# Kernel optimization log

Measured on AMD Instinct MI355X. Metric: run time of the kernel, lower is better.

Reference implementation:

```python
import jax, jax.numpy as jnp
import numpy as np

N_NODES = 100000
N_EDGES = 1200000
IN, HID, OUT = 64, 64, 32


def setup_inputs() -> dict:
    key = jax.random.key(0)
    ks = jax.random.split(key, 8)
    return {
        "features": jax.random.normal(ks[0], (N_NODES, IN), dtype=jnp.float32),
        "src": jax.random.randint(ks[1], (N_EDGES,), 0, N_NODES),
        "dst": jax.random.randint(ks[2], (N_EDGES,), 0, N_NODES),
        "W_self1": jax.random.normal(ks[3], (IN, HID), dtype=jnp.float32) / np.sqrt(IN),
        "W_neigh1": jax.random.normal(ks[4], (IN, HID), dtype=jnp.float32) / np.sqrt(IN),
        "b1": jnp.zeros((HID,), dtype=jnp.float32),
        "W_self2": jax.random.normal(ks[5], (HID, OUT), dtype=jnp.float32) / np.sqrt(HID),
        "W_neigh2": jax.random.normal(ks[6], (HID, OUT), dtype=jnp.float32) / np.sqrt(HID),
        "b2": jnp.zeros((OUT,), dtype=jnp.float32),
    }


def _sage_mean(h, src, dst, n_nodes, W_self, W_neigh, b):
    # DGL SAGEConv(mean): mean over in-neighbors' source features, then
    # rst = fc_self(h_dst) + fc_neigh(h_neigh) + bias
    msg = h[src]  # [E, d] irregular gather
    agg = jax.ops.segment_sum(msg, dst, num_segments=n_nodes)  # [N, d]
    deg = jax.ops.segment_sum(jnp.ones_like(dst, dtype=h.dtype), dst, num_segments=n_nodes)
    h_neigh = agg / jnp.maximum(deg, 1.0)[:, None]  # zero in-degree -> 0 (matches DGL)
    return h @ W_self + h_neigh @ W_neigh + b


def reference(features, src, dst, W_self1, W_neigh1, b1, W_self2, W_neigh2, b2):
    n = features.shape[0]
    # buffer.update is a distributed history-cache passthrough -> identity here
    h = _sage_mean(features, src, dst, n, W_self1, W_neigh1, b1)
    h = _sage_mean(h, src, dst, n, W_self2, W_neigh2, b2)
    return h
```

## Files before the change

### kernel.cpp

```cpp
#include <hip/hip_runtime.h>

constexpr int NN    = 100000;
constexpr int NE    = 1200000;

constexpr int NBUK = 196;
constexpr int PB   = 256;
constexpr int EPB  = (NE + PB - 1) / PB;
constexpr int MAT  = NBUK * PB;
constexpr int NBM  = (NN + 63) / 64;

typedef float  f32x4 __attribute__((ext_vector_type(4)));
typedef short  s16x8 __attribute__((ext_vector_type(8)));

static __device__ __forceinline__ unsigned short f2b(float f) {
    unsigned int u = __float_as_uint(f);
    u = (u + 0x7FFFu + ((u >> 16) & 1u)) >> 16;
    return (unsigned short)u;
}
static __device__ __forceinline__ float blo(unsigned int v) {
    return __uint_as_float(v << 16);
}
static __device__ __forceinline__ float bhi(unsigned int v) {
    return __uint_as_float(v & 0xFFFF0000u);
}

__global__ __launch_bounds__(256) void k_p1hist(const int* __restrict__ dst,
                                                int* __restrict__ mat) {
    __shared__ int h[NBUK];
    const int t = threadIdx.x, blk = blockIdx.x;
    for (int i = t; i < NBUK; i += 256) h[i] = 0;
    __syncthreads();
    int beg4 = blk * (EPB / 4);
    int end4 = beg4 + EPB / 4;
    if (end4 > NE / 4) end4 = NE / 4;
    for (int i = beg4 + t; i < end4; i += 256) {
        const int4 d = ((const int4*)dst)[i];
        atomicAdd(&h[d.x >> 9], 1);
        atomicAdd(&h[d.y >> 9], 1);
        atomicAdd(&h[d.z >> 9], 1);
        atomicAdd(&h[d.w >> 9], 1);
    }
    __syncthreads();
    for (int b = t; b < NBUK; b += 256) mat[b * PB + blk] = h[b];
}

__global__ __launch_bounds__(256) void k_scanA(const int* __restrict__ mat,
                                               int* __restrict__ matX,
                                               int* __restrict__ T) {
    __shared__ int lds[256];
    const int b = blockIdx.x, t = threadIdx.x;
    int v = mat[b * 256 + t];
    lds[t] = v;
    __syncthreads();
    for (int d = 1; d < 256; d <<= 1) {
        int x = (t >= d) ? lds[t - d] : 0;
        __syncthreads();
        lds[t] += x;
        __syncthreads();
    }
    matX[b * 256 + t] = lds[t] - v;
    if (t == 255) T[b] = lds[255];
}

__global__ __launch_bounds__(256) void k_scanB(const int* __restrict__ T,
                                               int* __restrict__ matX) {
    __shared__ int lds[256];
    const int b = blockIdx.x, t = threadIdx.x;
    lds[t] = (t < NBUK) ? T[t] : 0;
    __syncthreads();
    for (int d = 1; d < 256; d <<= 1) {
        int x = (t >= d) ? lds[t - d] : 0;
        __syncthreads();
        lds[t] += x;
        __syncthreads();
    }
    int base = (b == 0) ? 0 : lds[b - 1];
    matX[b * 256 + t] += base;
    if (b == 0 && t == 0) matX[MAT] = NE;
}

__global__ __launch_bounds__(256) void k_p1place(const int* __restrict__ src,
                                                 const int* __restrict__ dst,
                                                 const int* __restrict__ matX,
                                                 unsigned int* __restrict__ P) {
    __shared__ int cur[NBUK];
    const int t = threadIdx.x, blk = blockIdx.x;
    for (int b = t; b < NBUK; b += 256) cur[b] = matX[b * PB + blk];
    __syncthreads();
    int beg4 = blk * (EPB / 4);
    int end4 = beg4 + EPB / 4;
    if (end4 > NE / 4) end4 = NE / 4;
    for (int i = beg4 + t; i < end4; i += 256) {
        const int4 d = ((const int4*)dst)[i];
        const int4 s = ((const int4*)src)[i];
        int p0 = atomicAdd(&cur[d.x >> 9], 1);
        int p1 = atomicAdd(&cur[d.y >> 9], 1);
        int p2 = atomicAdd(&cur[d.z >> 9], 1);
        int p3 = atomicAdd(&cur[d.w >> 9], 1);
        P[p0] = (unsigned)s.x | ((unsigned)(d.x & 511) << 17);
        P[p1] = (unsigned)s.y | ((unsigned)(d.y & 511) << 17);
        P[p2] = (unsigned)s.z | ((unsigned)(d.z & 511) << 17);
        P[p3] = (unsigned)s.w | ((unsigned)(d.w & 511) << 17);
    }
}

__global__ __launch_bounds__(256) void k_sort2_mfma1(const unsigned int* __restrict__ P,
                                                     const int* __restrict__ matX,
                                                     int* __restrict__ esrc,
                                                     int* __restrict__ off,
                                                     const float* __restrict__ feat,
                                                     const float* __restrict__ Ws,
                                                     const float* __restrict__ Wn,
                                                     const float* __restrict__ b,
                                                     unsigned short* __restrict__ C1) {
    __shared__ char smem[16384];
    const int tid = threadIdx.x;

    if (blockIdx.x < NBUK) {
        const int bb = blockIdx.x;
        int* cnt = (int*)smem;
        int* sA  = (int*)(smem + 2048);
        int* sB  = (int*)(smem + 4096);
        const int beg = matX[bb * PB];
        const int end = matX[(bb + 1) * PB];

        for (int i = tid; i < 512; i += 256) cnt[i] = 0;
        __syncthreads();
        for (int i = beg + tid; i < end; i += 256)
            atomicAdd(&cnt[P[i] >> 17], 1);
        __syncthreads();
        for (int i = tid; i < 512; i += 256) sA[i] = cnt[i];
        __syncthreads();
        int* pin = sA; int* pout = sB;
        for (int d = 1; d < 512; d <<= 1) {
            for (int i = tid; i < 512; i += 256)
                pout[i] = pin[i] + (i >= d ? pin[i - d] : 0);
            __syncthreads();
            int* tmp = pin; pin = pout; pout = tmp;
        }
        const int nodes = (bb == NBUK - 1) ? (NN - (NBUK - 1) * 512) : 512;
        for (int i = tid; i < 512; i += 256) {
            int ex = i ? pin[i - 1] : 0;
            cnt[i] = ex;
            if (i < nodes) off[bb * 512 + i] = beg + ex;
        }
        if (bb == NBUK - 1 && tid == 0) off[NN] = NE;
        __syncthreads();
        for (int i = beg + tid; i < end; i += 256) {
            unsigned v = P[i];
            int dl = (int)(v >> 17);
            int pos = atomicAdd(&cnt[dl], 1);
            esrc[beg + pos] = (int)(v & 0x1FFFFu);
        }
        return;
    }

    unsigned short* Bl = (unsigned short*)smem;
    const int mid = blockIdx.x - NBUK;

    for (int idx = tid; idx < 16 * 64; idx += 256) {
        int frag = idx >> 6, le = idx & 63;
        int ct = frag >> 1, kt = frag & 1;
        int col = ct * 16 + (le & 15);
        int kb  = kt * 32 + (le >> 4) * 8;
        unsigned short tmp[8];
#pragma unroll
        for (int j = 0; j < 8; ++j) {
            int k = kb + j;
            float w = (col < 64) ? Ws[k * 64 + col] : Wn[k * 64 + (col - 64)];
            tmp[j] = f2b(w);
        }
        uint4 pk;
        pk.x = (unsigned)tmp[0] | ((unsigned)tmp[1] << 16);
        pk.y = (unsigned)tmp[2] | ((unsigned)tmp[3] << 16);
        pk.z = (unsigned)tmp[4] | ((unsigned)tmp[5] << 16);
        pk.w = (unsigned)tmp[6] | ((unsigned)tmp[7] << 16);
        *(uint4*)(&Bl[idx * 8]) = pk;
    }
    __syncthreads();

    const int wave = tid >> 6, lane = tid & 63;
    const int r0 = mid * 64 + wave * 16;

    s16x8 a[2];
#pragma unroll
    for (int kt = 0; kt < 2; ++kt) {
        int row = r0 + (lane & 15);
        if (row >= NN) row = NN - 1;
        int kb = kt * 32 + (lane >> 4) * 8;
        const float4 f0 = *(const float4*)(feat + (size_t)row * 64 + kb);
        const float4 f1 = *(const float4*)(feat + (size_t)row * 64 + kb + 4);
        a[kt][0] = (short)f2b(f0.x); a[kt][1] = (short)f2b(f0.y);
        a[kt][2] = (short)f2b(f0.z); a[kt][3] = (short)f2b(f0.w);
        a[kt][4] = (short)f2b(f1.x); a[kt][5] = (short)f2b(f1.y);
        a[kt][6] = (short)f2b(f1.z); a[kt][7] = (short)f2b(f1.w);
    }

    const s16x8* Bl8 = (const s16x8*)Bl;
#pragma unroll
    for (int ct = 0; ct < 8; ++ct) {
        f32x4 acc = {0.f, 0.f, 0.f, 0.f};
#pragma unroll
        for (int kt = 0; kt < 2; ++kt) {
            s16x8 bf = Bl8[(ct * 2 + kt) * 64 + lane];
            acc = __builtin_amdgcn_mfma_f32_16x16x32_bf16(a[kt], bf, acc, 0, 0, 0);
        }
        int c = ct * 16 + (lane & 15);
        float bias = (c < 64) ? b[c] : 0.f;
#pragma unroll
        for (int q = 0; q < 4; ++q) {
            int r = r0 + (lane >> 4) * 4 + q;
            if (r < NN) C1[(size_t)r * 128 + c] = f2b(acc[q] + bias);
        }
    }
}

__global__ __launch_bounds__(256) void k_gath1_mfma2(const int* __restrict__ off,
                                                     const int* __restrict__ esrc,
                                                     const unsigned short* __restrict__ C1,
                                                     const float* __restrict__ Ws,
                                                     const float* __restrict__ Wn,
                                                     const float* __restrict__ b,
                                                     float* __restrict__ C2s,
                                                     unsigned short* __restrict__ C2n) {
    __shared__ unsigned short Bl[8 * 64 * 8];
    __shared__ unsigned short Hl[64 * 64];
    const int tid = threadIdx.x;

    for (int idx = tid; idx < 8 * 64; idx += 256) {
        int frag = idx >> 6, le = idx & 63;
        int ct = frag >> 1, kt = frag & 1;
        int col = ct * 16 + (le & 15);
        int kb  = kt * 32 + (le >> 4) * 8;
        unsigned short tmp[8];
#pragma unroll
        for (int j = 0; j < 8; ++j) {
            int k = kb + j;
            float w = (col < 32) ? Ws[k * 32 + col] : Wn[k * 32 + (col - 32)];
            tmp[j] = f2b(w);
        }
        uint4 pk;
        pk.x = (unsigned)tmp[0] | ((unsigned)tmp[1] << 16);
        pk.y = (unsigned)tmp[2] | ((unsigned)tmp[3] << 16);
        pk.z = (unsigned)tmp[4] | ((unsigned)tmp[5] << 16);
        pk.w = (unsigned)tmp[6] | ((unsigned)tmp[7] << 16);
        *(uint4*)(&Bl[idx * 8]) = pk;
    }

    const int base = blockIdx.x * 64;
    const int sub = tid & 7;
#pragma unroll 1
    for (int g = 0; g < 2; ++g) {
        int rloc = g * 32 + (tid >> 3);
        int node = base + rloc;
        if (node < NN) {
            int beg = off[node], end = off[node + 1];
            float a0 = 0.f, a1 = 0.f, a2 = 0.f, a3 = 0.f;
            float a4 = 0.f, a5 = 0.f, a6 = 0.f, a7 = 0.f;
            float c0 = 0.f, c1 = 0.f, c2 = 0.f, c3 = 0.f;
            float c4 = 0.f, c5 = 0.f, c6 = 0.f, c7 = 0.f;
            int k = beg;
            for (; k + 3 < end; k += 4) {
                int e0 = esrc[k], e1 = esrc[k + 1], e2 = esrc[k + 2], e3 = esrc[k + 3];
                uint4 v0 = *(const uint4*)(C1 + (size_t)e0 * 128 + 64 + sub * 8);
                uint4 v1 = *(const uint4*)(C1 + (size_t)e1 * 128 + 64 + sub * 8);
                uint4 v2 = *(const uint4*)(C1 + (size_t)e2 * 128 + 64 + sub * 8);
                uint4 v3 = *(const uint4*)(C1 + (size_t)e3 * 128 + 64 + sub * 8);
                a0 += blo(v0.x); a1 += bhi(v0.x); a2 += blo(v0.y); a3 += bhi(v0.y);
                a4 += blo(v0.z); a5 += bhi(v0.z); a6 += blo(v0.w); a7 += bhi(v0.w);
                c0 += blo(v1.x); c1 += bhi(v1.x); c2 += blo(v1.y); c3 += bhi(v1.y);
                c4 += blo(v1.z); c5 += bhi(v1.z); c6 += blo(v1.w); c7 += bhi(v1.w);
                a0 += blo(v2.x); a1 += bhi(v2.x); a2 += blo(v2.y); a3 += bhi(v2.y);
                a4 += blo(v2.z); a5 += bhi(v2.z); a6 += blo(v2.w); a7 += bhi(v2.w);
                c0 += blo(v3.x); c1 += bhi(v3.x); c2 += blo(v3.y); c3 += bhi(v3.y);
                c4 += blo(v3.z); c5 += bhi(v3.z); c6 += blo(v3.w); c7 += bhi(v3.w);
            }
            for (; k < end; ++k) {
                int e = esrc[k];
                uint4 v = *(const uint4*)(C1 + (size_t)e * 128 + 64 + sub * 8);
                a0 += blo(v.x); a1 += bhi(v.x); a2 += blo(v.y); a3 += bhi(v.y);
                a4 += blo(v.z); a5 += bhi(v.z); a6 += blo(v.w); a7 += bhi(v.w);
            }
            a0 += c0; a1 += c1; a2 += c2; a3 += c3;
            a4 += c4; a5 += c5; a6 += c6; a7 += c7;
            float inv = (end > beg) ? 1.0f / (float)(end - beg) : 0.f;
            uint4 sv = *(const uint4*)(C1 + (size_t)node * 128 + sub * 8);
            uint4 w;
            w.x = (unsigned)f2b(blo(sv.x) + a0 * inv) | ((unsigned)f2b(bhi(sv.x) + a1 * inv) << 16);
            w.y = (unsigned)f2b(blo(sv.y) + a2 * inv) | ((unsigned)f2b(bhi(sv.y) + a3 * inv) << 16);
            w.z = (unsigned)f2b(blo(sv.z) + a4 * inv) | ((unsigned)f2b(bhi(sv.z) + a5 * inv) << 16);
            w.w = (unsigned)f2b(blo(sv.w) + a6 * inv) | ((unsigned)f2b(bhi(sv.w) + a7 * inv) << 16);
            int boff = (rloc * 128 + sub * 16) ^ ((rloc & 7) << 4);
            *(uint4*)((char*)Hl + boff) = w;
        }
    }
    __syncthreads();

    const int wave = tid >> 6, lane = tid & 63;
    const int rl = wave * 16 + (lane & 15);

    s16x8 a[2];
#pragma unroll
    for (int kt = 0; kt < 2; ++kt) {
        int boff = rl * 128 + kt * 64 + (lane >> 4) * 16;
        a[kt] = *(const s16x8*)((const char*)Hl + (boff ^ ((rl & 7) << 4)));
    }

    const s16x8* Bl8 = (const s16x8*)Bl;
#pragma unroll
    for (int ct = 0; ct < 4; ++ct) {
        f32x4 acc = {0.f, 0.f, 0.f, 0.f};
#pragma unroll
        for (int kt = 0; kt < 2; ++kt) {
            s16x8 bf = Bl8[(ct * 2 + kt) * 64 + lane];
            acc = __builtin_amdgcn_mfma_f32_16x16x32_bf16(a[kt], bf, acc, 0, 0, 0);
        }
        int c = ct * 16 + (lane & 15);
#pragma unroll
        for (int q = 0; q < 4; ++q) {
            int r = blockIdx.x * 64 + wave * 16 + (lane >> 4) * 4 + q;
            if (r < NN) {
                if (c < 32) C2s[(size_t)r * 32 + c] = acc[q] + b[c];
                else        C2n[(size_t)r * 32 + (c - 32)] = f2b(acc[q]);
            }
        }
    }
}

__global__ __launch_bounds__(256) void k_gath2(const int* __restrict__ off,
                                               const int* __restrict__ esrc,
                                               const float* __restrict__ C2s,
                                               const unsigned short* __restrict__ C2n,
                                               float* __restrict__ out) {
    int node = blockIdx.x * 64 + (threadIdx.x >> 2);
    int sub  = threadIdx.x & 3;
    if (node >= NN) return;
    int beg = off[node], end = off[node + 1];
    float a0 = 0.f, a1 = 0.f, a2 = 0.f, a3 = 0.f;
    float a4 = 0.f, a5 = 0.f, a6 = 0.f, a7 = 0.f;
    float c0 = 0.f, c1 = 0.f, c2 = 0.f, c3 = 0.f;
    float c4 = 0.f, c5 = 0.f, c6 = 0.f, c7 = 0.f;
    int k = beg;
    for (; k + 3 < end; k += 4) {
        int e0 = esrc[k], e1 = esrc[k + 1], e2 = esrc[k + 2], e3 = esrc[k + 3];
        uint4 v0 = *(const uint4*)(C2n + (size_t)e0 * 32 + sub * 8);
        uint4 v1 = *(const uint4*)(C2n + (size_t)e1 * 32 + sub * 8);
        uint4 v2 = *(const uint4*)(C2n + (size_t)e2 * 32 + sub * 8);
        uint4 v3 = *(const uint4*)(C2n + (size_t)e3 * 32 + sub * 8);
        a0 += blo(v0.x); a1 += bhi(v0.x); a2 += blo(v0.y); a3 += bhi(v0.y);
        a4 += blo(v0.z); a5 += bhi(v0.z); a6 += blo(v0.w); a7 += bhi(v0.w);
        c0 += blo(v1.x); c1 += bhi(v1.x); c2 += blo(v1.y); c3 += bhi(v1.y);
        c4 += blo(v1.z); c5 += bhi(v1.z); c6 += blo(v1.w); c7 += bhi(v1.w);
        a0 += blo(v2.x); a1 += bhi(v2.x); a2 += blo(v2.y); a3 += bhi(v2.y);
        a4 += blo(v2.z); a5 += bhi(v2.z); a6 += blo(v2.w); a7 += bhi(v2.w);
        c0 += blo(v3.x); c1 += bhi(v3.x); c2 += blo(v3.y); c3 += bhi(v3.y);
        c4 += blo(v3.z); c5 += bhi(v3.z); c6 += blo(v3.w); c7 += bhi(v3.w);
    }
    for (; k < end; ++k) {
        int e = esrc[k];
        uint4 v = *(const uint4*)(C2n + (size_t)e * 32 + sub * 8);
        a0 += blo(v.x); a1 += bhi(v.x); a2 += blo(v.y); a3 += bhi(v.y);
        a4 += blo(v.z); a5 += bhi(v.z); a6 += blo(v.w); a7 += bhi(v.w);
    }
    a0 += c0; a1 += c1; a2 += c2; a3 += c3;
    a4 += c4; a5 += c5; a6 += c6; a7 += c7;
    float inv = (end > beg) ? 1.0f / (float)(end - beg) : 0.f;
    const float4 s0 = *(const float4*)(C2s + (size_t)node * 32 + sub * 8);
    const float4 s1 = *(const float4*)(C2s + (size_t)node * 32 + sub * 8 + 4);
    float4 o0, o1;
    o0.x = s0.x + a0 * inv; o0.y = s0.y + a1 * inv;
    o0.z = s0.z + a2 * inv; o0.w = s0.w + a3 * inv;
    o1.x = s1.x + a4 * inv; o1.y = s1.y + a5 * inv;
    o1.z = s1.z + a6 * inv; o1.w = s1.w + a7 * inv;
    *(float4*)(out + (size_t)node * 32 + sub * 8) = o0;
    *(float4*)(out + (size_t)node * 32 + sub * 8 + 4) = o1;
}

extern "C" void kernel_launch(void* const* d_in, const int* in_sizes, int n_in,
                              void* d_out, int out_size, void* d_ws, size_t ws_size,
                              hipStream_t stream) {
    const float* feat    = (const float*)d_in[0];
    const int*   src     = (const int*)d_in[1];
    const int*   dst     = (const int*)d_in[2];
    const float* Wself1  = (const float*)d_in[3];
    const float* Wneigh1 = (const float*)d_in[4];
    const float* b1      = (const float*)d_in[5];
    const float* Wself2  = (const float*)d_in[6];
    const float* Wneigh2 = (const float*)d_in[7];
    const float* b2      = (const float*)d_in[8];
    float* out = (float*)d_out;

    char* ws = (char*)d_ws;
    size_t offb = 0;
    auto alloc = [&](size_t bytes) -> void* {
        void* p = ws + offb;
        offb += (bytes + 255) & ~(size_t)255;
        return p;
    };
    int*            mat  = (int*)alloc((size_t)MAT * sizeof(int));
    int*            matX = (int*)alloc((size_t)(MAT + 1) * sizeof(int));
    int*            T    = (int*)alloc(256 * sizeof(int));
    unsigned int*   P    = (unsigned int*)alloc((size_t)NE * sizeof(int));
    int*            esrc = (int*)alloc((size_t)NE * sizeof(int));
    int*            off  = (int*)alloc((size_t)(NN + 1) * sizeof(int));
    unsigned short* C1   = (unsigned short*)alloc((size_t)NN * 128 * 2);
    float*          C2s  = (float*)alloc((size_t)NN * 32 * sizeof(float));
    unsigned short* C2n  = (unsigned short*)alloc((size_t)NN * 32 * 2);

    k_p1hist<<<PB, 256, 0, stream>>>(dst, mat);
    k_scanA<<<NBUK, 256, 0, stream>>>(mat, matX, T);
    k_scanB<<<NBUK, 256, 0, stream>>>(T, matX);
    k_p1place<<<PB, 256, 0, stream>>>(src, dst, matX, P);

    k_sort2_mfma1<<<NBUK + NBM, 256, 0, stream>>>(P, matX, esrc, off,
                                                  feat, Wself1, Wneigh1, b1, C1);

    k_gath1_mfma2<<<(NN + 63) / 64, 256, 0, stream>>>(off, esrc, C1, Wself2, Wneigh2, b2, C2s, C2n);
    k_gath2<<<(NN + 63) / 64, 256, 0, stream>>>(off, esrc, C2s, C2n, out);
}
```

Before: 97.07 us.

## Spread layer-1 MFMA tiles across sort-stage kernels and merge two-pass scan

```diff
diff --git a/kernel.cpp b/kernel.cpp
--- a/kernel.cpp
+++ b/kernel.cpp
@@ -9,6 +9,11 @@
 constexpr int MAT  = NBUK * PB;
 constexpr int NBM  = (NN + 63) / 64;
 
+constexpr int M_HIST  = 473;
+constexpr int M_SCAN  = 150;
+constexpr int M_PLACE = 470;
+constexpr int M_SORT  = NBM - M_HIST - M_SCAN - M_PLACE;
+
 typedef float  f32x4 __attribute__((ext_vector_type(4)));
 typedef short  s16x8 __attribute__((ext_vector_type(8)));
 
@@ -24,140 +29,13 @@
     return __uint_as_float(v & 0xFFFF0000u);
 }
 
-__global__ __launch_bounds__(256) void k_p1hist(const int* __restrict__ dst,
-                                                int* __restrict__ mat) {
-    __shared__ int h[NBUK];
-    const int t = threadIdx.x, blk = blockIdx.x;
-    for (int i = t; i < NBUK; i += 256) h[i] = 0;
-    __syncthreads();
-    int beg4 = blk * (EPB / 4);
-    int end4 = beg4 + EPB / 4;
-    if (end4 > NE / 4) end4 = NE / 4;
-    for (int i = beg4 + t; i < end4; i += 256) {
-        const int4 d = ((const int4*)dst)[i];
-        atomicAdd(&h[d.x >> 9], 1);
-        atomicAdd(&h[d.y >> 9], 1);
-        atomicAdd(&h[d.z >> 9], 1);
-        atomicAdd(&h[d.w >> 9], 1);
-    }
-    __syncthreads();
-    for (int b = t; b < NBUK; b += 256) mat[b * PB + blk] = h[b];
-}
-
-__global__ __launch_bounds__(256) void k_scanA(const int* __restrict__ mat,
-                                               int* __restrict__ matX,
-                                               int* __restrict__ T) {
-    __shared__ int lds[256];
-    const int b = blockIdx.x, t = threadIdx.x;
-    int v = mat[b * 256 + t];
-    lds[t] = v;
-    __syncthreads();
-    for (int d = 1; d < 256; d <<= 1) {
-        int x = (t >= d) ? lds[t - d] : 0;
-        __syncthreads();
-        lds[t] += x;
-        __syncthreads();
-    }
-    matX[b * 256 + t] = lds[t] - v;
-    if (t == 255) T[b] = lds[255];
-}
-
-__global__ __launch_bounds__(256) void k_scanB(const int* __restrict__ T,
-                                               int* __restrict__ matX) {
-    __shared__ int lds[256];
-    const int b = blockIdx.x, t = threadIdx.x;
-    lds[t] = (t < NBUK) ? T[t] : 0;
-    __syncthreads();
-    for (int d = 1; d < 256; d <<= 1) {
-        int x = (t >= d) ? lds[t - d] : 0;
-        __syncthreads();
-        lds[t] += x;
-        __syncthreads();
-    }
-    int base = (b == 0) ? 0 : lds[b - 1];
-    matX[b * 256 + t] += base;
-    if (b == 0 && t == 0) matX[MAT] = NE;
-}
-
-__global__ __launch_bounds__(256) void k_p1place(const int* __restrict__ src,
-                                                 const int* __restrict__ dst,
-                                                 const int* __restrict__ matX,
-                                                 unsigned int* __restrict__ P) {
-    __shared__ int cur[NBUK];
-    const int t = threadIdx.x, blk = blockIdx.x;
-    for (int b = t; b < NBUK; b += 256) cur[b] = matX[b * PB + blk];
-    __syncthreads();
-    int beg4 = blk * (EPB / 4);
-    int end4 = beg4 + EPB / 4;
-    if (end4 > NE / 4) end4 = NE / 4;
-    for (int i = beg4 + t; i < end4; i += 256) {
-        const int4 d = ((const int4*)dst)[i];
-        const int4 s = ((const int4*)src)[i];
-        int p0 = atomicAdd(&cur[d.x >> 9], 1);
-        int p1 = atomicAdd(&cur[d.y >> 9], 1);
-        int p2 = atomicAdd(&cur[d.z >> 9], 1);
-        int p3 = atomicAdd(&cur[d.w >> 9], 1);
-        P[p0] = (unsigned)s.x | ((unsigned)(d.x & 511) << 17);
-        P[p1] = (unsigned)s.y | ((unsigned)(d.y & 511) << 17);
-        P[p2] = (unsigned)s.z | ((unsigned)(d.z & 511) << 17);
-        P[p3] = (unsigned)s.w | ((unsigned)(d.w & 511) << 17);
-    }
-}
-
-__global__ __launch_bounds__(256) void k_sort2_mfma1(const unsigned int* __restrict__ P,
-                                                     const int* __restrict__ matX,
-                                                     int* __restrict__ esrc,
-                                                     int* __restrict__ off,
-                                                     const float* __restrict__ feat,
-                                                     const float* __restrict__ Ws,
-                                                     const float* __restrict__ Wn,
-                                                     const float* __restrict__ b,
-                                                     unsigned short* __restrict__ C1) {
-    __shared__ char smem[16384];
-    const int tid = threadIdx.x;
-
-    if (blockIdx.x < NBUK) {
-        const int bb = blockIdx.x;
-        int* cnt = (int*)smem;
-        int* sA  = (int*)(smem + 2048);
-        int* sB  = (int*)(smem + 4096);
-        const int beg = matX[bb * PB];
-        const int end = matX[(bb + 1) * PB];
-
-        for (int i = tid; i < 512; i += 256) cnt[i] = 0;
-        __syncthreads();
-        for (int i = beg + tid; i < end; i += 256)
-            atomicAdd(&cnt[P[i] >> 17], 1);
-        __syncthreads();
-        for (int i = tid; i < 512; i += 256) sA[i] = cnt[i];
-        __syncthreads();
-        int* pin = sA; int* pout = sB;
-        for (int d = 1; d < 512; d <<= 1) {
-            for (int i = tid; i < 512; i += 256)
-                pout[i] = pin[i] + (i >= d ? pin[i - d] : 0);
-            __syncthreads();
-            int* tmp = pin; pin = pout; pout = tmp;
-        }
-        const int nodes = (bb == NBUK - 1) ? (NN - (NBUK - 1) * 512) : 512;
-        for (int i = tid; i < 512; i += 256) {
-            int ex = i ? pin[i - 1] : 0;
-            cnt[i] = ex;
-            if (i < nodes) off[bb * 512 + i] = beg + ex;
-        }
-        if (bb == NBUK - 1 && tid == 0) off[NN] = NE;
-        __syncthreads();
-        for (int i = beg + tid; i < end; i += 256) {
-            unsigned v = P[i];
-            int dl = (int)(v >> 17);
-            int pos = atomicAdd(&cnt[dl], 1);
-            esrc[beg + pos] = (int)(v & 0x1FFFFu);
-        }
-        return;
-    }
-
+static __device__ __forceinline__ void mfma1_tile(int mid, int tid, char* smem,
+                                                  const float* __restrict__ feat,
+                                                  const float* __restrict__ Ws,
+                                                  const float* __restrict__ Wn,
+                                                  const float* __restrict__ bias,
+                                                  unsigned short* __restrict__ C1) {
     unsigned short* Bl = (unsigned short*)smem;
-    const int mid = blockIdx.x - NBUK;
-
     for (int idx = tid; idx < 16 * 64; idx += 256) {
         int frag = idx >> 6, le = idx & 63;
         int ct = frag >> 1, kt = frag & 1;
@@ -206,13 +84,176 @@
             acc = __builtin_amdgcn_mfma_f32_16x16x32_bf16(a[kt], bf, acc, 0, 0, 0);
         }
         int c = ct * 16 + (lane & 15);
-        float bias = (c < 64) ? b[c] : 0.f;
+        float bv = (c < 64) ? bias[c] : 0.f;
 #pragma unroll
         for (int q = 0; q < 4; ++q) {
             int r = r0 + (lane >> 4) * 4 + q;
-            if (r < NN) C1[(size_t)r * 128 + c] = f2b(acc[q] + bias);
-        }
-    }
+            if (r < NN) C1[(size_t)r * 128 + c] = f2b(acc[q] + bv);
+        }
+    }
+}
+
+__global__ __launch_bounds__(256) void k_p1hist(const int* __restrict__ dst,
+                                                int* __restrict__ mat,
+                                                const float* __restrict__ feat,
+                                                const float* __restrict__ Ws,
+                                                const float* __restrict__ Wn,
+                                                const float* __restrict__ bias,
+                                                unsigned short* __restrict__ C1) {
+    __shared__ char smem[16384];
+    const int tid = threadIdx.x;
+    if (blockIdx.x < PB) {
+        int* h = (int*)smem;
+        const int blk = blockIdx.x;
+        for (int i = tid; i < NBUK; i += 256) h[i] = 0;
+        __syncthreads();
+        int beg4 = blk * (EPB / 4);
+        int end4 = beg4 + EPB / 4;
+        if (end4 > NE / 4) end4 = NE / 4;
+        for (int i = beg4 + tid; i < end4; i += 256) {
+            const int4 d = ((const int4*)dst)[i];
+            atomicAdd(&h[d.x >> 9], 1);
+            atomicAdd(&h[d.y >> 9], 1);
+            atomicAdd(&h[d.z >> 9], 1);
+            atomicAdd(&h[d.w >> 9], 1);
+        }
+        __syncthreads();
+        for (int b = tid; b < NBUK; b += 256) mat[b * PB + blk] = h[b];
+        return;
+    }
+    mfma1_tile(blockIdx.x - PB, tid, smem, feat, Ws, Wn, bias, C1);
+}
+
+__global__ __launch_bounds__(256) void k_scanAB(const int* __restrict__ mat,
+                                                int* __restrict__ matX,
+                                                const float* __restrict__ feat,
+                                                const float* __restrict__ Ws,
+                                                const float* __restrict__ Wn,
+                                                const float* __restrict__ bias,
+                                                unsigned short* __restrict__ C1) {
+    __shared__ char smem[16384];
+    const int tid = threadIdx.x;
+    if (blockIdx.x < NBUK) {
+        int* lds = (int*)smem;
+        const int bb = blockIdx.x;
+        int part = 0;
+        int r = 0;
+        for (; r + 3 < bb; r += 4)
+            part += mat[r * 256 + tid] + mat[(r + 1) * 256 + tid]
+                  + mat[(r + 2) * 256 + tid] + mat[(r + 3) * 256 + tid];
+        for (; r < bb; ++r) part += mat[r * 256 + tid];
+        lds[tid] = part;
+        __syncthreads();
+        for (int w = 128; w > 0; w >>= 1) {
+            if (tid < w) lds[tid] += lds[tid + w];
+            __syncthreads();
+        }
+        const int base = lds[0];
+        __syncthreads();
+        int v = mat[bb * 256 + tid];
+        lds[tid] = v;
+        __syncthreads();
+        for (int d = 1; d < 256; d <<= 1) {
+            int x = (tid >= d) ? lds[tid - d] : 0;
+            __syncthreads();
+            lds[tid] += x;
+            __syncthreads();
+        }
+        matX[bb * 256 + tid] = base + lds[tid] - v;
+        if (bb == 0 && tid == 0) matX[MAT] = NE;
+        return;
+    }
+    mfma1_tile(M_HIST + blockIdx.x - NBUK, tid, smem, feat, Ws, Wn, bias, C1);
+}
+
+__global__ __launch_bounds__(256) void k_p1place(const int* __restrict__ src,
+                                                 const int* __restrict__ dst,
+                                                 const int* __restrict__ matX,
+                                                 unsigned int* __restrict__ P,
+                                                 const float* __restrict__ feat,
+                                                 const float* __restrict__ Ws,
+                                                 const float* __restrict__ Wn,
+                                                 const float* __restrict__ bias,
+                                                 unsigned short* __restrict__ C1) {
+    __shared__ char smem[16384];
+    const int tid = threadIdx.x;
+    if (blockIdx.x < PB) {
+        int* cur = (int*)smem;
+        const int blk = blockIdx.x;
+        for (int b = tid; b < NBUK; b += 256) cur[b] = matX[b * PB + blk];
+        __syncthreads();
+        int beg4 = blk * (EPB / 4);
+        int end4 = beg4 + EPB / 4;
+        if (end4 > NE / 4) end4 = NE / 4;
+        for (int i = beg4 + tid; i < end4; i += 256) {
+            const int4 d = ((const int4*)dst)[i];
+            const int4 s = ((const int4*)src)[i];
+            int p0 = atomicAdd(&cur[d.x >> 9], 1);
+            int p1 = atomicAdd(&cur[d.y >> 9], 1);
+            int p2 = atomicAdd(&cur[d.z >> 9], 1);
+            int p3 = atomicAdd(&cur[d.w >> 9], 1);
+            P[p0] = (unsigned)s.x | ((unsigned)(d.x & 511) << 17);
+            P[p1] = (unsigned)s.y | ((unsigned)(d.y & 511) << 17);
+            P[p2] = (unsigned)s.z | ((unsigned)(d.z & 511) << 17);
+            P[p3] = (unsigned)s.w | ((unsigned)(d.w & 511) << 17);
+        }
+        return;
+    }
+    mfma1_tile(M_HIST + M_SCAN + blockIdx.x - PB, tid, smem, feat, Ws, Wn, bias, C1);
+}
+
+__global__ __launch_bounds__(256) void k_sort2(const unsigned int* __restrict__ P,
+                                               const int* __restrict__ matX,
+                                               int* __restrict__ esrc,
+                                               int* __restrict__ off,
+                                               const float* __restrict__ feat,
+                                               const float* __restrict__ Ws,
+                                               const float* __restrict__ Wn,
+                                               const float* __restrict__ bias,
+                                               unsigned short* __restrict__ C1) {
+    __shared__ char smem[16384];
+    const int tid = threadIdx.x;
+
+    if (blockIdx.x < NBUK) {
+        const int bb = blockIdx.x;
+        int* cnt = (int*)smem;
+        int* sA  = (int*)(smem + 2048);
+        int* sB  = (int*)(smem + 4096);
+        const int beg = matX[bb * PB];
+        const int end = matX[(bb + 1) * PB];
+
+        for (int i = tid; i < 512; i += 256) cnt[i] = 0;
+        __syncthreads();
+        for (int i = beg + tid; i < end; i += 256)
+            atomicAdd(&cnt[P[i] >> 17], 1);
+        __syncthreads();
+        for (int i = tid; i < 512; i += 256) sA[i] = cnt[i];
+        __syncthreads();
+        int* pin = sA; int* pout = sB;
+        for (int d = 1; d < 512; d <<= 1) {
+            for (int i = tid; i < 512; i += 256)
+                pout[i] = pin[i] + (i >= d ? pin[i - d] : 0);
+            __syncthreads();
+            int* tmp = pin; pin = pout; pout = tmp;
+        }
+        const int nodes = (bb == NBUK - 1) ? (NN - (NBUK - 1) * 512) : 512;
+        for (int i = tid; i < 512; i += 256) {
+            int ex = i ? pin[i - 1] : 0;
+            cnt[i] = ex;
+            if (i < nodes) off[bb * 512 + i] = beg + ex;
+        }
+        if (bb == NBUK - 1 && tid == 0) off[NN] = NE;
+        __syncthreads();
+        for (int i = beg + tid; i < end; i += 256) {
+            unsigned v = P[i];
+            int dl = (int)(v >> 17);
+            int pos = atomicAdd(&cnt[dl], 1);
+            esrc[beg + pos] = (int)(v & 0x1FFFFu);
+        }
+        return;
+    }
+    mfma1_tile(M_HIST + M_SCAN + M_PLACE + blockIdx.x - NBUK, tid, smem,
+               feat, Ws, Wn, bias, C1);
 }
 
 __global__ __launch_bounds__(256) void k_gath1_mfma2(const int* __restrict__ off,
@@ -399,7 +440,6 @@
     };
     int*            mat  = (int*)alloc((size_t)MAT * sizeof(int));
     int*            matX = (int*)alloc((size_t)(MAT + 1) * sizeof(int));
-    int*            T    = (int*)alloc(256 * sizeof(int));
     unsigned int*   P    = (unsigned int*)alloc((size_t)NE * sizeof(int));
     int*            esrc = (int*)alloc((size_t)NE * sizeof(int));
     int*            off  = (int*)alloc((size_t)(NN + 1) * sizeof(int));
@@ -407,13 +447,12 @@
     float*          C2s  = (float*)alloc((size_t)NN * 32 * sizeof(float));
     unsigned short* C2n  = (unsigned short*)alloc((size_t)NN * 32 * 2);
 
-    k_p1hist<<<PB, 256, 0, stream>>>(dst, mat);
-    k_scanA<<<NBUK, 256, 0, stream>>>(mat, matX, T);
-    k_scanB<<<NBUK, 256, 0, stream>>>(T, matX);
-    k_p1place<<<PB, 256, 0, stream>>>(src, dst, matX, P);
-
-    k_sort2_mfma1<<<NBUK + NBM, 256, 0, stream>>>(P, matX, esrc, off,
-                                                  feat, Wself1, Wneigh1, b1, C1);
+    k_p1hist<<<PB + M_HIST, 256, 0, stream>>>(dst, mat, feat, Wself1, Wneigh1, b1, C1);
+    k_scanAB<<<NBUK + M_SCAN, 256, 0, stream>>>(mat, matX, feat, Wself1, Wneigh1, b1, C1);
+    k_p1place<<<PB + M_PLACE, 256, 0, stream>>>(src, dst, matX, P,
+                                                feat, Wself1, Wneigh1, b1, C1);
+    k_sort2<<<NBUK + M_SORT, 256, 0, stream>>>(P, matX, esrc, off,
+                                               feat, Wself1, Wneigh1, b1, C1);
 
     k_gath1_mfma2<<<(NN + 63) / 64, 256, 0, stream>>>(off, esrc, C1, Wself2, Wneigh2, b2, C2s, C2n);
     k_gath2<<<(NN + 63) / 64, 256, 0, stream>>>(off, esrc, C2s, C2n, out);
```

New measurement: 107.8 us. +11.0%, slower.
